# Performance work log

Measured on AMD Instinct MI355X. Metric: run time of the kernel, lower is better.

Reference implementation:

```python
import jax, jax.numpy as jnp
import numpy as np
import math

B, S, E, H, F = 2, 2048, 1024, 16, 4096
D = E // H
EPS = 1e-5


def _layernorm(x, g, b):
    mu = jnp.mean(x, axis=-1, keepdims=True)
    var = jnp.mean(jnp.square(x - mu), axis=-1, keepdims=True)
    return (x - mu) * jax.lax.rsqrt(var + EPS) * g + b


def _xavier(k, fan_in, fan_out):
    limit = math.sqrt(6.0 / (fan_in + fan_out))
    return jax.random.uniform(k, (fan_in, fan_out), jnp.float32, -limit, limit)


def setup_inputs() -> dict:
    key = jax.random.key(0)
    ks = jax.random.split(key, 8)
    x = jax.random.normal(ks[0], (B, S, E), jnp.float32)
    # causal mask: 1 where attendable, 0 where masked (masked_fill at mask==0)
    mask = jnp.tril(jnp.ones((S, S), jnp.int32))[None, None]  # [1,1,S,S]
    return {
        "x": x,
        "mask": mask,
        "Wq": _xavier(ks[1], E, E), "bq": jnp.zeros((E,), jnp.float32),
        "Wk": _xavier(ks[2], E, E), "bk": jnp.zeros((E,), jnp.float32),
        "Wv": _xavier(ks[3], E, E), "bv": jnp.zeros((E,), jnp.float32),
        "Wo": _xavier(ks[4], E, E), "bo": jnp.zeros((E,), jnp.float32),
        "W1": _xavier(ks[5], E, F), "b1": jnp.zeros((F,), jnp.float32),
        "W2": _xavier(ks[6], F, E), "b2": jnp.zeros((E,), jnp.float32),
        "ln1_g": jnp.ones((E,), jnp.float32), "ln1_b": jnp.zeros((E,), jnp.float32),
        "ln2_g": jnp.ones((E,), jnp.float32), "ln2_b": jnp.zeros((E,), jnp.float32),
    }


def reference(x, mask, Wq, bq, Wk, bk, Wv, bv, Wo, bo, W1, b1, W2, b2,
              ln1_g, ln1_b, ln2_g, ln2_b):
    n = _layernorm(x, ln1_g, ln1_b)
    # project and split heads: [B,S,E] -> [B,H,S,D]
    def heads(w, b):
        return (n @ w + b).reshape(B, S, H, D).transpose(0, 2, 1, 3)
    Q, K, V = heads(Wq, bq), heads(Wk, bk), heads(Wv, bv)
    scores = jnp.einsum('bhsd,bhtd->bhst', Q, K) / math.sqrt(D)  # [B,H,S,S]
    scores = jnp.where(mask == 0, jnp.float32(-1e9), scores)
    attn = jax.nn.softmax(scores, axis=-1)
    ctx = jnp.einsum('bhst,bhtd->bhsd', attn, V)
    ctx = ctx.transpose(0, 2, 1, 3).reshape(B, S, E)
    attn_out = ctx @ Wo + bo
    x = _layernorm(x + attn_out, ln2_g, ln2_b)
    ffn = jax.nn.gelu(x @ W1 + b1, approximate=False) @ W2 + b2
    return x + ffn
```

## Files before the change

kernel.cpp:

```cpp
#include <hip/hip_runtime.h>
#include <cmath>

typedef unsigned short u16;
typedef unsigned int u32;
typedef __bf16 bf16x8 __attribute__((ext_vector_type(8)));
typedef float f32x4 __attribute__((ext_vector_type(4)));

#define SEQ 2048
#define EMB 1024
#define NHEAD 16
#define HDIM 64
#define FFDIM 4096
#define NBATCH 2
#define QKVLD 3072
#define PWS 68

#define QSCALE 0.18033688011112042f

__device__ __forceinline__ u16 f2bf(float f) {
  u32 u = __float_as_uint(f);
  u32 r = u + 0x7fffu + ((u >> 16) & 1u);
  return (u16)(r >> 16);
}

__device__ __forceinline__ float ex2(float x) {
#if __has_builtin(__builtin_amdgcn_exp2f)
  return __builtin_amdgcn_exp2f(x);
#else
  return exp2f(x);
#endif
}

__device__ __forceinline__ float geluf(float x) {
  float u = 0.7978845608028654f * (x + 0.044715f * x * x * x);
  float e = ex2(2.8853900817779268f * u);
  return x - x / (e + 1.0f);
}

__device__ __forceinline__ void gload16(const void* g, void* l) {
  __builtin_amdgcn_global_load_lds(
      (const __attribute__((address_space(1))) unsigned int*)g,
      (__attribute__((address_space(3))) unsigned int*)l, 16, 0, 0);
}

__device__ __forceinline__ u32 lds_addr(const void* p) {
  return (u32)(size_t)(const __attribute__((address_space(3))) void*)p;
}

template <int IMM>
__device__ __forceinline__ bf16x8 dsr16(u32 a) {
  bf16x8 r;
  asm volatile("ds_read_b128 %0, %1 offset:%2" : "=v"(r) : "v"(a), "n"(IMM));
  return r;
}

__device__ __forceinline__ void xcd_swizzle(int gx, int gy, int& bx, int& by) {
  int nwg = gx * gy;
  int lin = blockIdx.x + gx * blockIdx.y;
  int q = nwg >> 3;
  int nl = (lin & 7) * q + (lin >> 3);
  bx = nl % gx;
  by = nl / gx;
}

template <int TX>
__device__ __forceinline__ void xcd_tile_swizzle(int gx, int gy, int& bx, int& by) {
  int nwg = gx * gy;
  int lin = blockIdx.x + gx * blockIdx.y;
  int c = lin & 7;
  int wdx = lin >> 3;
  int q = nwg >> 3;
  int TY = q / TX;
  int ncx = gx / TX;
  int xt = c % ncx, yt = c / ncx;
  bx = xt * TX + wdx % TX;
  by = yt * TY + wdx / TX;
}

__global__ __launch_bounds__(256)
void wtrans_kernel(const float* __restrict__ W, u16* __restrict__ WT, int K, int N) {
  __shared__ float tile[32][33];
  int tx = threadIdx.x & 31, ty = threadIdx.x >> 5;
  int n0 = blockIdx.x * 32, k0 = blockIdx.y * 32;
#pragma unroll
  for (int i = 0; i < 32; i += 8)
    tile[ty + i][tx] = W[(size_t)(k0 + ty + i) * N + (n0 + tx)];
  __syncthreads();
#pragma unroll
  for (int i = 0; i < 32; i += 8)
    WT[(size_t)(n0 + ty + i) * K + (k0 + tx)] = f2bf(tile[tx][ty + i]);
}

__global__ __launch_bounds__(256)
void wtrans4_kernel(const float* __restrict__ W0, const float* __restrict__ W1_,
                    const float* __restrict__ W2_, const float* __restrict__ W3,
                    u16* __restrict__ Dqkv, u16* __restrict__ Do) {
  __shared__ float tile[32][33];
  int z = blockIdx.z;
  const float* W = (z == 0) ? W0 : (z == 1) ? W1_ : (z == 2) ? W2_ : W3;
  u16* D = (z < 3) ? (Dqkv + (size_t)z * EMB * EMB) : Do;
  int tx = threadIdx.x & 31, ty = threadIdx.x >> 5;
  int n0 = blockIdx.x * 32, k0 = blockIdx.y * 32;
#pragma unroll
  for (int i = 0; i < 32; i += 8)
    tile[ty + i][tx] = W[(size_t)(k0 + ty + i) * EMB + (n0 + tx)];
  __syncthreads();
#pragma unroll
  for (int i = 0; i < 32; i += 8)
    D[(size_t)(n0 + ty + i) * EMB + (k0 + tx)] = f2bf(tile[tx][ty + i]);
}

__global__ __launch_bounds__(256)
void vtrans_kernel(const u16* __restrict__ QKV, u16* __restrict__ Vt) {
  __shared__ u16 tile[64 * 72];
  int bh = blockIdx.y, b = bh >> 4, h = bh & 15;
  int s0 = blockIdx.x * 64;
  const u16* src = QKV + (size_t)b * SEQ * QKVLD + 2048 + (size_t)h * HDIM;
  int tid = threadIdx.x;
#pragma unroll
  for (int cc = 0; cc < 2; ++cc) {
    int c = tid + cc * 256;
    int s = c >> 3, d0 = (c & 7) * 8;
    uint4 v = *(const uint4*)(src + (size_t)(s0 + s) * QKVLD + d0);
    *(uint4*)(&tile[s * 72 + d0]) = v;
  }
  __syncthreads();
  u16* dst = Vt + (size_t)bh * HDIM * SEQ;
#pragma unroll
  for (int cc = 0; cc < 2; ++cc) {
    int c = tid + cc * 256;
    int d = c >> 3, t0l = (c & 7) * 8;
    union { uint4 u; u16 s[8]; } ou;
#pragma unroll
    for (int j = 0; j < 8; ++j) ou.s[j] = tile[(t0l + j) * 72 + d];
    *(uint4*)(dst + (size_t)d * SEQ + s0 + t0l) = ou.u;
  }
}

__global__ __launch_bounds__(256)
void ln_kernel(const float* __restrict__ in, const float* __restrict__ gamma,
               const float* __restrict__ beta, u16* __restrict__ outb) {
  int w = threadIdx.x >> 6, lane = threadIdx.x & 63;
  int row = blockIdx.x * 4 + w;
  size_t base = (size_t)row * EMB;
  float4 v[4];
  float s = 0.f, q = 0.f;
#pragma unroll
  for (int j = 0; j < 4; ++j) {
    v[j] = *(const float4*)(in + base + j * 256 + lane * 4);
    s += v[j].x + v[j].y + v[j].z + v[j].w;
    q += v[j].x * v[j].x + v[j].y * v[j].y + v[j].z * v[j].z + v[j].w * v[j].w;
  }
#pragma unroll
  for (int off = 1; off < 64; off <<= 1) {
    s += __shfl_xor(s, off);
    q += __shfl_xor(q, off);
  }
  float mean = s * (1.0f / EMB);
  float var = q * (1.0f / EMB) - mean * mean;
  float rstd = rsqrtf(var + 1e-5f);
#pragma unroll
  for (int j = 0; j < 4; ++j) {
    int c = j * 256 + lane * 4;
    float4 g4 = *(const float4*)(gamma + c);
    float4 b4 = *(const float4*)(beta + c);
    ushort4 ob;
    ob.x = f2bf((v[j].x - mean) * rstd * g4.x + b4.x);
    ob.y = f2bf((v[j].y - mean) * rstd * g4.y + b4.y);
    ob.z = f2bf((v[j].z - mean) * rstd * g4.z + b4.z);
    ob.w = f2bf((v[j].w - mean) * rstd * g4.w + b4.w);
    *(ushort4*)(outb + base + c) = ob;
  }
}

__global__ __launch_bounds__(256)
void ln2f_kernel(const float* __restrict__ p, size_t pstride,
                 const float* __restrict__ bias, const float* __restrict__ resid,
                 const float* __restrict__ gamma, const float* __restrict__ beta,
                 u16* __restrict__ outb, float* __restrict__ outf) {
  int w = threadIdx.x >> 6, lane = threadIdx.x & 63;
  int row = blockIdx.x * 4 + w;
  size_t base = (size_t)row * EMB;
  float4 v[4];
  float s = 0.f, q = 0.f;
#pragma unroll
  for (int j = 0; j < 4; ++j) {
    int c = j * 256 + lane * 4;
    float4 a = *(const float4*)(p + base + c);
    float4 b = *(const float4*)(p + pstride + base + c);
    float4 r = *(const float4*)(resid + base + c);
    float4 bb = *(const float4*)(bias + c);
    v[j].x = a.x + b.x + r.x + bb.x;
    v[j].y = a.y + b.y + r.y + bb.y;
    v[j].z = a.z + b.z + r.z + bb.z;
    v[j].w = a.w + b.w + r.w + bb.w;
    s += v[j].x + v[j].y + v[j].z + v[j].w;
    q += v[j].x * v[j].x + v[j].y * v[j].y + v[j].z * v[j].z + v[j].w * v[j].w;
  }
#pragma unroll
  for (int off = 1; off < 64; off <<= 1) {
    s += __shfl_xor(s, off);
    q += __shfl_xor(q, off);
  }
  float mean = s * (1.0f / EMB);
  float var = q * (1.0f / EMB) - mean * mean;
  float rstd = rsqrtf(var + 1e-5f);
#pragma unroll
  for (int j = 0; j < 4; ++j) {
    int c = j * 256 + lane * 4;
    float4 g4 = *(const float4*)(gamma + c);
    float4 b4 = *(const float4*)(beta + c);
    float y0 = (v[j].x - mean) * rstd * g4.x + b4.x;
    float y1 = (v[j].y - mean) * rstd * g4.y + b4.y;
    float y2 = (v[j].z - mean) * rstd * g4.z + b4.z;
    float y3 = (v[j].w - mean) * rstd * g4.w + b4.w;
    ushort4 ob;
    ob.x = f2bf(y0); ob.y = f2bf(y1); ob.z = f2bf(y2); ob.w = f2bf(y3);
    *(ushort4*)(outb + base + c) = ob;
    *(float4*)(outf + base + c) = make_float4(y0, y1, y2, y3);
  }
}

__global__ __launch_bounds__(256)
void reduce2_kernel(const float* __restrict__ p, size_t pstride,
                    const float* __restrict__ bias, const float* __restrict__ resid,
                    float* __restrict__ out, int ncols) {
  size_t i = ((size_t)blockIdx.x * 256 + threadIdx.x) * 4;
  float4 a = *(const float4*)(p + i);
  float4 b = *(const float4*)(p + pstride + i);
  float4 r = *(const float4*)(resid + i);
  int col = (int)(i & (size_t)(ncols - 1));
  float4 bb = *(const float4*)(bias + col);
  float4 o;
  o.x = a.x + b.x + r.x + bb.x;
  o.y = a.y + b.y + r.y + bb.y;
  o.z = a.z + b.z + r.z + bb.z;
  o.w = a.w + b.w + r.w + bb.w;
  *(float4*)(out + i) = o;
}

__global__ __launch_bounds__(256)
void gemm_bt(const u16* __restrict__ A, const u16* __restrict__ BT,
             const float* __restrict__ bias, const float* __restrict__ bias2,
             const float* __restrict__ bias3, void* __restrict__ out,
             const float* __restrict__ resid, int M, int N, int K,
             int mode, float scale, int ksplit,
             float* __restrict__ partial, size_t pstride) {
  __shared__ __align__(16) u16 As[128 * 64];
  __shared__ __align__(16) u16 Bs[128 * 64];
  int tid = threadIdx.x;
  int lane = tid & 63, w = tid >> 6;
  int wm = w >> 1, wn = w & 1;
  int g = lane >> 4, lr = lane & 15;
  int bx, by;
  xcd_swizzle(gridDim.x, gridDim.y, bx, by);
  int m0 = by * 128, n0 = bx * 128;
  int z = blockIdx.z;
  int kbeg = z * ksplit, kend = kbeg + ksplit;

  f32x4 acc[4][4];
#pragma unroll
  for (int mt = 0; mt < 4; ++mt)
#pragma unroll
    for (int nt = 0; nt < 4; ++nt) {
      acc[mt][nt][0] = 0.f; acc[mt][nt][1] = 0.f;
      acc[mt][nt][2] = 0.f; acc[mt][nt][3] = 0.f;
    }

  size_t ao[4], bo_[4];
  int lo[4];
#pragma unroll
  for (int cc = 0; cc < 4; ++cc) {
    int c = tid + cc * 256;
    int row = c >> 3, slot = c & 7;
    int gc = slot ^ (row & 7);
    ao[cc] = (size_t)(m0 + row) * K + gc * 8;
    bo_[cc] = (size_t)(n0 + row) * K + gc * 8;
    lo[cc] = c * 8;
  }
  int swz[2];
#pragma unroll
  for (int kk = 0; kk < 2; ++kk) swz[kk] = ((kk * 4 + g) ^ (lr & 7)) * 8;

  for (int k0 = kbeg; k0 < kend; k0 += 64) {
    __syncthreads();
#pragma unroll
    for (int cc = 0; cc < 4; ++cc) gload16(A + ao[cc] + k0, As + lo[cc]);
#pragma unroll
    for (int cc = 0; cc < 4; ++cc) gload16(BT + bo_[cc] + k0, Bs + lo[cc]);
    __syncthreads();
#pragma unroll
    for (int kk = 0; kk < 2; ++kk) {
      bf16x8 af[4], bfr[4];
#pragma unroll
      for (int mt = 0; mt < 4; ++mt)
        af[mt] = *(const bf16x8*)(As + (wm * 64 + mt * 16 + lr) * 64 + swz[kk]);
#pragma unroll
      for (int nt = 0; nt < 4; ++nt)
        bfr[nt] = *(const bf16x8*)(Bs + (wn * 64 + nt * 16 + lr) * 64 + swz[kk]);
#pragma unroll
      for (int mt = 0; mt < 4; ++mt)
#pragma unroll
        for (int nt = 0; nt < 4; ++nt)
          acc[mt][nt] = __builtin_amdgcn_mfma_f32_16x16x32_bf16(af[mt], bfr[nt], acc[mt][nt], 0, 0, 0);
    }
  }

  float* pz = partial + (size_t)z * pstride;
#pragma unroll
  for (int mt = 0; mt < 4; ++mt) {
    int row = m0 + wm * 64 + mt * 16 + g * 4;
#pragma unroll
    for (int nt = 0; nt < 4; ++nt) {
      int col = n0 + wn * 64 + nt * 16 + lr;
      float bcol;
      if (mode == 3) {
        int which = col >> 10;
        const float* bp = (which == 0) ? bias : (which == 1) ? bias2 : bias3;
        bcol = bp[col & 1023];
      } else if (mode != 4) {
        bcol = bias[col];
      } else {
        bcol = 0.f;
      }
#pragma unroll
      for (int r = 0; r < 4; ++r) {
        float vacc = acc[mt][nt][r] + bcol;
        size_t idx = (size_t)(row + r) * N + col;
        if (mode == 0)      ((u16*)out)[idx] = f2bf(vacc * scale);
        else if (mode == 1) ((u16*)out)[idx] = f2bf(geluf(vacc));
        else if (mode == 2) ((float*)out)[idx] = vacc + resid[idx];
        else if (mode == 3) ((u16*)out)[idx] = f2bf(col < 1024 ? vacc * QSCALE : vacc);
        else                pz[idx] = vacc;
      }
    }
  }
}


#define BARM __builtin_amdgcn_s_barrier()
#define VMW6 asm volatile("s_waitcnt vmcnt(6)")
#define VMW0 asm volatile("s_waitcnt vmcnt(0)")
#define NOSTG ((void)0)
#define NOWT ((void)0)
#define NABUF (128 * 32)

#define STGN_A(t, d, kh)                                                      \
  { gload16(A + (size_t)sgA[0] + kbeg + (t) * 64 + (kh) * 32,                 \
            As + ((d) * 2 + (kh)) * NABUF + sl[0]);                           \
    gload16(A + (size_t)sgA[1] + kbeg + (t) * 64 + (kh) * 32,                 \
            As + ((d) * 2 + (kh)) * NABUF + sl[1]); }

#define STGN_B(t, d, kh)                                                      \
  { gload16(BT + (size_t)sgB[0] + kbeg + (t) * 64 + (kh) * 32,                \
            Bs + ((d) * 2 + (kh)) * NABUF + sl[0]);                           \
    gload16(BT + (size_t)sgB[1] + kbeg + (t) * 64 + (kh) * 32,                \
            Bs + ((d) * 2 + (kh)) * NABUF + sl[1]); }

#define PHASEN(d, kk, mh, STAGE, WAITC)                                       \
  {                                                                           \
    const u32 bA = bB + ((d) * 2 + (kk)) * (NABUF * 2);                       \
    const u32 aA = aB + ((d) * 2 + (kk)) * (NABUF * 2);                       \
    if ((mh) == 0) {                                                          \
      bfr[0] = dsr16<0>(bA);                                                  \
      bfr[1] = dsr16<1024>(bA);                                               \
      bfr[2] = dsr16<2048>(bA);                                               \
      bfr[3] = dsr16<3072>(bA);                                               \
    }                                                                         \
    bf16x8 af[2];                                                             \
    af[0] = dsr16<(((mh) * 2 + 0) * 1024)>(aA);                               \
    af[1] = dsr16<(((mh) * 2 + 1) * 1024)>(aA);                               \
    STAGE;                                                                    \
    BARM;                                                                     \
    asm volatile("s_waitcnt lgkmcnt(0)");                                     \
    __builtin_amdgcn_sched_barrier(0);                                        \
    __builtin_amdgcn_s_setprio(1);                                            \
    _Pragma("unroll")                                                         \
    for (int mi = 0; mi < 2; ++mi)                                            \
      _Pragma("unroll")                                                       \
      for (int nt = 0; nt < 4; ++nt)                                          \
        acc[(mh) * 2 + mi][nt] = __builtin_amdgcn_mfma_f32_16x16x32_bf16(     \
            af[mi], bfr[nt], acc[(mh) * 2 + mi][nt], 0, 0, 0);                \
    __builtin_amdgcn_s_setprio(0);                                            \
    WAITC;                                                                    \
    BARM;                                                                     \
  }

template <int TXS>
__global__ __launch_bounds__(256, 2)
void gemm8n(const u16* __restrict__ A, const u16* __restrict__ BT,
            const float* __restrict__ bias, const float* __restrict__ bias2,
            const float* __restrict__ bias3, void* __restrict__ out,
            const float* __restrict__ resid, int M, int N, int K,
            int mode, float scale, int ksplit,
            float* __restrict__ partial, size_t pstride) {
  __shared__ __align__(16) u16 As[4 * NABUF];
  __shared__ __align__(16) u16 Bs[4 * NABUF];
  int tid = threadIdx.x;
  int lane = tid & 63, w = tid >> 6;
  int wm = w >> 1, wn = w & 1;
  int g = lane >> 4, lr = lane & 15;
  int bx, by;
  xcd_tile_swizzle<TXS>(gridDim.x, gridDim.y, bx, by);
  int m0 = by * 128, n0 = bx * 128;
  int z = blockIdx.z;
  size_t kbeg = (size_t)z * ksplit;
  int nk = ksplit >> 6, npair = nk >> 1;

  int phys = ((lr & 1) * 4 + g) ^ ((lr >> 1) & 7);
  int aoff = wm * 64 * 32 + (lr >> 1) * 64 + phys * 8;
  int boff = wn * 64 * 32 + (lr >> 1) * 64 + phys * 8;
  const u32 aB = lds_addr(As) + 2 * aoff;
  const u32 bB = lds_addr(Bs) + 2 * boff;

  int sgA[2], sgB[2], sl[2];
#pragma unroll
  for (int j = 0; j < 2; ++j) {
    int c = tid + j * 256;
    int sr = c >> 3, ph = c & 7, l = ph ^ (sr & 7);
    sgA[j] = (m0 + 2 * sr + (l >> 2)) * K + (l & 3) * 8;
    sgB[j] = (n0 + 2 * sr + (l >> 2)) * K + (l & 3) * 8;
    sl[j] = c * 8;
  }

  f32x4 acc[4][4];
#pragma unroll
  for (int mt = 0; mt < 4; ++mt)
#pragma unroll
    for (int nt = 0; nt < 4; ++nt) {
      acc[mt][nt][0] = 0.f; acc[mt][nt][1] = 0.f;
      acc[mt][nt][2] = 0.f; acc[mt][nt][3] = 0.f;
    }

  bf16x8 bfr[4];

  STGN_B(0, 0, 0); STGN_A(0, 0, 0); STGN_B(0, 0, 1); STGN_A(0, 0, 1);
  STGN_B(1, 1, 0); STGN_A(1, 1, 0); STGN_B(1, 1, 1);
  VMW6; BARM;

  for (int it = 0; it < npair - 1; ++it) {
    int t1 = 2 * it + 1, t2 = 2 * it + 2, t3 = 2 * it + 3;
    PHASEN(0, 0, 0, STGN_A(t1, 1, 1), NOWT)
    PHASEN(0, 0, 1, STGN_B(t2, 0, 0), NOWT)
    PHASEN(0, 1, 0, STGN_A(t2, 0, 0), NOWT)
    PHASEN(0, 1, 1, STGN_B(t2, 0, 1), VMW6)
    PHASEN(1, 0, 0, STGN_A(t2, 0, 1), NOWT)
    PHASEN(1, 0, 1, STGN_B(t3, 1, 0), NOWT)
    PHASEN(1, 1, 0, STGN_A(t3, 1, 0), NOWT)
    PHASEN(1, 1, 1, STGN_B(t3, 1, 1), VMW6)
  }
  {
    int t1 = nk - 1;
    PHASEN(0, 0, 0, STGN_A(t1, 1, 1), NOWT)
    PHASEN(0, 0, 1, NOSTG, NOWT)
    PHASEN(0, 1, 0, NOSTG, NOWT)
    PHASEN(0, 1, 1, NOSTG, VMW0)
    PHASEN(1, 0, 0, NOSTG, NOWT)
    PHASEN(1, 0, 1, NOSTG, NOWT)
    PHASEN(1, 1, 0, NOSTG, NOWT)
    PHASEN(1, 1, 1, NOSTG, NOWT)
  }

  float* pz = partial + (size_t)z * pstride;
#pragma unroll
  for (int mt = 0; mt < 4; ++mt) {
    int row = m0 + wm * 64 + mt * 16 + g * 4;
#pragma unroll
    for (int nt = 0; nt < 4; ++nt) {
      int col = n0 + wn * 64 + nt * 16 + lr;
      float bcol;
      if (mode == 3) {
        int which = col >> 10;
        const float* bp = (which == 0) ? bias : (which == 1) ? bias2 : bias3;
        bcol = bp[col & 1023];
      } else if (mode != 4) {
        bcol = bias[col];
      } else {
        bcol = 0.f;
      }
#pragma unroll
      for (int r = 0; r < 4; ++r) {
        float vacc = acc[mt][nt][r] + bcol;
        size_t idx = (size_t)(row + r) * N + col;
        if (mode == 0)      ((u16*)out)[idx] = f2bf(vacc * scale);
        else if (mode == 1) ((u16*)out)[idx] = f2bf(geluf(vacc));
        else if (mode == 2) ((float*)out)[idx] = vacc + resid[idx];
        else if (mode == 3) ((u16*)out)[idx] = f2bf(col < 1024 ? vacc * QSCALE : vacc);
        else                pz[idx] = vacc;
      }
    }
  }
}

__shared__ __align__(16) u16 attn_Kt[64 * 64];
__shared__ __align__(16) u16 attn_VT[64 * 64];
__shared__ __align__(16) u16 attn_Pw[2][4][16 * PWS];

template <int S0>
__device__ __forceinline__ void attn_tile(
    int t0, const int* q0, int w, int g, int lr, const bf16x8& ones,
    bf16x8 (&qf)[2][2], f32x4 (&lacc)[2], f32x4 (&oacc)[2][4]) {
  f32x4 sacc[2][4];
#pragma unroll
  for (int s = S0; s < 2; ++s)
#pragma unroll
    for (int nt = 0; nt < 4; ++nt) {
      sacc[s][nt][0] = 0.f; sacc[s][nt][1] = 0.f;
      sacc[s][nt][2] = 0.f; sacc[s][nt][3] = 0.f;
    }
#pragma unroll
  for (int kk = 0; kk < 2; ++kk)
#pragma unroll
    for (int nt = 0; nt < 4; ++nt) {
      int sw = ((kk * 4 + g) ^ lr) & 7;
      bf16x8 bfr = *(const bf16x8*)(&attn_Kt[(nt * 16 + lr) * 64 + sw * 8]);
      if (S0 == 0)
        sacc[0][nt] = __builtin_amdgcn_mfma_f32_16x16x32_bf16(qf[0][kk], bfr, sacc[0][nt], 0, 0, 0);
      sacc[1][nt] = __builtin_amdgcn_mfma_f32_16x16x32_bf16(qf[1][kk], bfr, sacc[1][nt], 0, 0, 0);
    }

#pragma unroll
  for (int s = S0; s < 2; ++s) {
    bool diag = (t0 == q0[s]);
#pragma unroll
    for (int r = 0; r < 4; ++r) {
#pragma unroll
      for (int nt = 0; nt < 4; ++nt) {
        float pv = ex2(sacc[s][nt][r]);
        if (diag && (nt * 16 + lr > w * 16 + g * 4 + r)) pv = 0.f;
        attn_Pw[s][w][(g * 4 + r) * PWS + nt * 16 + lr] = f2bf(pv);
      }
    }
  }

#pragma unroll
  for (int kk = 0; kk < 2; ++kk) {
    bf16x8 pf0, pf1;
    if (S0 == 0) pf0 = *(const bf16x8*)(&attn_Pw[0][w][lr * PWS + kk * 32 + g * 8]);
    pf1 = *(const bf16x8*)(&attn_Pw[1][w][lr * PWS + kk * 32 + g * 8]);
#pragma unroll
    for (int nt = 0; nt < 4; ++nt) {
      int sw = ((kk * 4 + g) ^ lr) & 7;
      bf16x8 vf = *(const bf16x8*)(&attn_VT[(nt * 16 + lr) * 64 + sw * 8]);
      if (S0 == 0)
        oacc[0][nt] = __builtin_amdgcn_mfma_f32_16x16x32_bf16(pf0, vf, oacc[0][nt], 0, 0, 0);
      oacc[1][nt] = __builtin_amdgcn_mfma_f32_16x16x32_bf16(pf1, vf, oacc[1][nt], 0, 0, 0);
    }
    if (S0 == 0)
      lacc[0] = __builtin_amdgcn_mfma_f32_16x16x32_bf16(pf0, ones, lacc[0], 0, 0, 0);
    lacc[1] = __builtin_amdgcn_mfma_f32_16x16x32_bf16(pf1, ones, lacc[1], 0, 0, 0);
  }
}

__global__ __launch_bounds__(256)
void attn2_kernel(const u16* __restrict__ QKV, const u16* __restrict__ Vt,
                  u16* __restrict__ ctx) {
  int tid = threadIdx.x, lane = tid & 63, w = tid >> 6;
  int g = lane >> 4, lr = lane & 15;
  int bh = blockIdx.y, b = bh >> 4, h = bh & 15;
  int q0[2];
  q0[0] = blockIdx.x * 64;
  q0[1] = (SEQ / 64 - 1 - blockIdx.x) * 64;
  const u16* Qh = QKV + (size_t)b * SEQ * QKVLD + (size_t)h * HDIM;
  const u16* Kh = Qh + 1024;
  const u16* Vth = Vt + (size_t)bh * HDIM * SEQ;

  bf16x8 ones;
#pragma unroll
  for (int j = 0; j < 8; ++j) ones[j] = (__bf16)1.0f;

  bf16x8 qf[2][2];
#pragma unroll
  for (int s = 0; s < 2; ++s)
#pragma unroll
    for (int kk = 0; kk < 2; ++kk)
      qf[s][kk] = *(const bf16x8*)(Qh + (size_t)(q0[s] + w * 16 + lr) * QKVLD + kk * 32 + g * 8);

  f32x4 lacc[2];
  f32x4 oacc[2][4];
#pragma unroll
  for (int s = 0; s < 2; ++s) {
    lacc[s][0] = 0.f; lacc[s][1] = 0.f; lacc[s][2] = 0.f; lacc[s][3] = 0.f;
#pragma unroll
    for (int nt = 0; nt < 4; ++nt) {
      oacc[s][nt][0] = 0.f; oacc[s][nt][1] = 0.f;
      oacc[s][nt][2] = 0.f; oacc[s][nt][3] = 0.f;
    }
  }

  int c1 = tid, c2 = tid + 256;
  int t1 = c1 >> 3, ch1 = (c1 ^ t1) & 7;
  int t2 = c2 >> 3, ch2 = (c2 ^ t2) & 7;
  for (int t0 = 0; t0 <= q0[1]; t0 += 64) {
    __syncthreads();
    gload16(Kh + (size_t)(t0 + t1) * QKVLD + ch1 * 8, attn_Kt + c1 * 8);
    gload16(Kh + (size_t)(t0 + t2) * QKVLD + ch2 * 8, attn_Kt + c2 * 8);
    gload16(Vth + (size_t)t1 * SEQ + t0 + ch1 * 8, attn_VT + c1 * 8);
    gload16(Vth + (size_t)t2 * SEQ + t0 + ch2 * 8, attn_VT + c2 * 8);
    __syncthreads();

    if (t0 <= q0[0])
      attn_tile<0>(t0, q0, w, g, lr, ones, qf, lacc, oacc);
    else
      attn_tile<1>(t0, q0, w, g, lr, ones, qf, lacc, oacc);
  }

#pragma unroll
  for (int s = 0; s < 2; ++s) {
    int srow = q0[s] + w * 16 + g * 4;
    float inv[4];
#pragma unroll
    for (int r = 0; r < 4; ++r) inv[r] = 1.0f / lacc[s][r];
#pragma unroll
    for (int nt = 0; nt < 4; ++nt) {
      int col = h * HDIM + nt * 16 + lr;
#pragma unroll
      for (int r = 0; r < 4; ++r) {
        float o = oacc[s][nt][r] * inv[r];
        ctx[((size_t)b * SEQ + srow + r) * EMB + col] = f2bf(o);
      }
    }
  }
}

extern "C" void kernel_launch(void* const* d_in, const int* in_sizes, int n_in,
                              void* d_out, int out_size, void* d_ws, size_t ws_size,
                              hipStream_t stream) {
  const float* x    = (const float*)d_in[0];
  const float* Wq   = (const float*)d_in[2];
  const float* bq   = (const float*)d_in[3];
  const float* Wk   = (const float*)d_in[4];
  const float* bk   = (const float*)d_in[5];
  const float* Wv   = (const float*)d_in[6];
  const float* bv   = (const float*)d_in[7];
  const float* Wo   = (const float*)d_in[8];
  const float* bo   = (const float*)d_in[9];
  const float* W1   = (const float*)d_in[10];
  const float* b1   = (const float*)d_in[11];
  const float* W2   = (const float*)d_in[12];
  const float* b2   = (const float*)d_in[13];
  const float* ln1g = (const float*)d_in[14];
  const float* ln1b = (const float*)d_in[15];
  const float* ln2g = (const float*)d_in[16];
  const float* ln2b = (const float*)d_in[17];

  char* ws = (char*)d_ws;
  u16* WqkvT = (u16*)(ws + ((size_t)0 << 20));
  u16* WoT   = (u16*)(ws + ((size_t)6 << 20));
  u16* W1T   = (u16*)(ws + ((size_t)8 << 20));
  u16* W2T   = (u16*)(ws + ((size_t)16 << 20));
  u16* xb    = (u16*)(ws + ((size_t)24 << 20));
  u16* QKVb  = (u16*)(ws + ((size_t)32 << 20));
  u16* ctxb  = (u16*)(ws + ((size_t)56 << 20));
  float* x2f = (float*)(ws + ((size_t)48 << 20));
  u16* x2b   = xb;
  u16* VtG   = (u16*)(ws + ((size_t)64 << 20));
  float* pWo = (float*)(ws + ((size_t)64 << 20));
  u16* h1    = (u16*)(ws + ((size_t)64 << 20));
  float* pF2 = (float*)(ws + ((size_t)0 << 20));

  dim3 blk(256);
  const int M = NBATCH * SEQ;

  wtrans4_kernel<<<dim3(32, 32, 4), blk, 0, stream>>>(Wq, Wk, Wv, Wo, WqkvT, WoT);
  wtrans_kernel<<<dim3(128, 32), blk, 0, stream>>>(W1, W1T, EMB, FFDIM);
  wtrans_kernel<<<dim3(32, 128), blk, 0, stream>>>(W2, W2T, FFDIM, EMB);

  ln_kernel<<<M / 4, blk, 0, stream>>>(x, ln1g, ln1b, xb);

  gemm_bt<<<dim3(QKVLD / 128, M / 128), blk, 0, stream>>>(
      xb, WqkvT, bq, bk, bv, QKVb, nullptr, M, QKVLD, EMB, 3, 1.0f, EMB, nullptr, 0);

  vtrans_kernel<<<dim3(SEQ / 64, NBATCH * NHEAD), blk, 0, stream>>>(QKVb, VtG);

  attn2_kernel<<<dim3(SEQ / 128, NBATCH * NHEAD), blk, 0, stream>>>(QKVb, VtG, ctxb);

  gemm8n<4><<<dim3(EMB / 128, M / 128, 2), blk, 0, stream>>>(
      ctxb, WoT, nullptr, nullptr, nullptr, nullptr, nullptr, M, EMB, EMB, 4, 1.0f,
      EMB / 2, pWo, (size_t)4 << 20);

  ln2f_kernel<<<M / 4, blk, 0, stream>>>(pWo, (size_t)4 << 20, bo, x, ln2g, ln2b,
                                         x2b, x2f);

  gemm8n<8><<<dim3(FFDIM / 128, M / 128), blk, 0, stream>>>(
      x2b, W1T, b1, nullptr, nullptr, h1, nullptr, M, FFDIM, EMB, 1, 1.0f, EMB,
      nullptr, 0);

  gemm8n<4><<<dim3(EMB / 128, M / 128, 2), blk, 0, stream>>>(
      h1, W2T, nullptr, nullptr, nullptr, nullptr, nullptr, M, EMB, FFDIM, 4, 1.0f,
      FFDIM / 2, pF2, (size_t)8 << 20);
  reduce2_kernel<<<M * EMB / 1024, blk, 0, stream>>>(pF2, (size_t)8 << 20, b2, x2f,
                                                     (float*)d_out, EMB);
}
```

Baseline: 404.9 us.

## Replace 128x128 GEMM with 512-thread 256-wide tile GEMM and coarser phases

Replaces the 256-thread 128x128 gemm8n with a templated 512-thread gemm4p using 128x256 or 256x256 output tiles and 8 waves. Each phase now loads all A fragments and computes the full per-wave tile, so there are four barrier phases per k-pair instead of eight. The goal is more reuse per LDS byte and fewer barriers for the Wo, FFN1 and FFN2 GEMMs. In exchange, grids get smaller and use plain xcd_swizzle instead of the tile swizzle. LDS use and register pressure also rise (64 accumulators per wave at BM=256), which may cut occupancy and wave counts.

```diff
diff --git a/kernel.cpp b/kernel.cpp
--- a/kernel.cpp
+++ b/kernel.cpp
@@ -61,20 +61,6 @@
   int nl = (lin & 7) * q + (lin >> 3);
   bx = nl % gx;
   by = nl / gx;
-}
-
-template <int TX>
-__device__ __forceinline__ void xcd_tile_swizzle(int gx, int gy, int& bx, int& by) {
-  int nwg = gx * gy;
-  int lin = blockIdx.x + gx * blockIdx.y;
-  int c = lin & 7;
-  int wdx = lin >> 3;
-  int q = nwg >> 3;
-  int TY = q / TX;
-  int ncx = gx / TX;
-  int xt = c % ncx, yt = c / ncx;
-  bx = xt * TX + wdx % TX;
-  by = yt * TY + wdx / TX;
 }
 
 __global__ __launch_bounds__(256)
@@ -339,93 +325,112 @@
 
 
 #define BARM __builtin_amdgcn_s_barrier()
-#define VMW6 asm volatile("s_waitcnt vmcnt(6)")
-#define VMW0 asm volatile("s_waitcnt vmcnt(0)")
 #define NOSTG ((void)0)
 #define NOWT ((void)0)
-#define NABUF (128 * 32)
-
-#define STGN_A(t, d, kh)                                                      \
-  { gload16(A + (size_t)sgA[0] + kbeg + (t) * 64 + (kh) * 32,                 \
-            As + ((d) * 2 + (kh)) * NABUF + sl[0]);                           \
-    gload16(A + (size_t)sgA[1] + kbeg + (t) * 64 + (kh) * 32,                 \
-            As + ((d) * 2 + (kh)) * NABUF + sl[1]); }
-
-#define STGN_B(t, d, kh)                                                      \
-  { gload16(BT + (size_t)sgB[0] + kbeg + (t) * 64 + (kh) * 32,                \
-            Bs + ((d) * 2 + (kh)) * NABUF + sl[0]);                           \
-    gload16(BT + (size_t)sgB[1] + kbeg + (t) * 64 + (kh) * 32,                \
-            Bs + ((d) * 2 + (kh)) * NABUF + sl[1]); }
-
-#define PHASEN(d, kk, mh, STAGE, WAITC)                                       \
+
+#define STG_A(t, d, kh)                                                       \
+  { _Pragma("unroll")                                                         \
+    for (int j = 0; j < RA; ++j)                                              \
+      gload16(A + (size_t)sgA[j] + kbeg + (t) * 64 + (kh) * 32,               \
+              As + ((d) * 2 + (kh)) * ABUF + slA[j]); }
+
+#define STG_B(t, d, kh)                                                       \
+  { _Pragma("unroll")                                                         \
+    for (int j = 0; j < 2; ++j)                                               \
+      gload16(BT + (size_t)sgB[j] + kbeg + (t) * 64 + (kh) * 32,              \
+              Bs + ((d) * 2 + (kh)) * 8192 + slB[j]); }
+
+#define STG_R(t, d, kh) { STG_B(t, d, kh); STG_A(t, d, kh); }
+
+#define VM2L asm volatile("s_waitcnt vmcnt(%0)" ::"n"(2 * (RA + 2)))
+#define VM1L asm volatile("s_waitcnt vmcnt(%0)" ::"n"(RA + 2))
+#define VMW0 asm volatile("s_waitcnt vmcnt(0)")
+
+#define PHASE4(d, kk, STAGE, WAITC)                                           \
   {                                                                           \
-    const u32 bA = bB + ((d) * 2 + (kk)) * (NABUF * 2);                       \
-    const u32 aA = aB + ((d) * 2 + (kk)) * (NABUF * 2);                       \
-    if ((mh) == 0) {                                                          \
-      bfr[0] = dsr16<0>(bA);                                                  \
-      bfr[1] = dsr16<1024>(bA);                                               \
-      bfr[2] = dsr16<2048>(bA);                                               \
-      bfr[3] = dsr16<3072>(bA);                                               \
+    const u32 bA = bB + ((d) * 2 + (kk)) * 16384;                             \
+    const u32 aA = aB + ((d) * 2 + (kk)) * (ABUF * 2);                        \
+    bfr[0] = dsr16<0>(bA);                                                    \
+    bfr[1] = dsr16<1024>(bA);                                                 \
+    bfr[2] = dsr16<2048>(bA);                                                 \
+    bfr[3] = dsr16<3072>(bA);                                                 \
+    bf16x8 af[MT];                                                            \
+    af[0] = dsr16<0>(aA);                                                     \
+    af[1] = dsr16<1024>(aA);                                                  \
+    af[2] = dsr16<2048>(aA);                                                  \
+    af[3] = dsr16<3072>(aA);                                                  \
+    if constexpr (MT > 4) {                                                   \
+      af[4] = dsr16<4096>(aA);                                                \
+      af[5] = dsr16<5120>(aA);                                                \
+      af[6] = dsr16<6144>(aA);                                                \
+      af[7] = dsr16<7168>(aA);                                                \
     }                                                                         \
-    bf16x8 af[2];                                                             \
-    af[0] = dsr16<(((mh) * 2 + 0) * 1024)>(aA);                               \
-    af[1] = dsr16<(((mh) * 2 + 1) * 1024)>(aA);                               \
     STAGE;                                                                    \
-    BARM;                                                                     \
     asm volatile("s_waitcnt lgkmcnt(0)");                                     \
     __builtin_amdgcn_sched_barrier(0);                                        \
     __builtin_amdgcn_s_setprio(1);                                            \
     _Pragma("unroll")                                                         \
-    for (int mi = 0; mi < 2; ++mi)                                            \
+    for (int mi = 0; mi < MT; ++mi)                                           \
       _Pragma("unroll")                                                       \
       for (int nt = 0; nt < 4; ++nt)                                          \
-        acc[(mh) * 2 + mi][nt] = __builtin_amdgcn_mfma_f32_16x16x32_bf16(     \
-            af[mi], bfr[nt], acc[(mh) * 2 + mi][nt], 0, 0, 0);                \
+        acc[mi][nt] = __builtin_amdgcn_mfma_f32_16x16x32_bf16(                \
+            af[mi], bfr[nt], acc[mi][nt], 0, 0, 0);                           \
     __builtin_amdgcn_s_setprio(0);                                            \
     WAITC;                                                                    \
     BARM;                                                                     \
   }
 
-template <int TXS>
-__global__ __launch_bounds__(256, 2)
-void gemm8n(const u16* __restrict__ A, const u16* __restrict__ BT,
+template <int BM>
+__global__ __launch_bounds__(512, 2)
+void gemm4p(const u16* __restrict__ A, const u16* __restrict__ BT,
             const float* __restrict__ bias, const float* __restrict__ bias2,
             const float* __restrict__ bias3, void* __restrict__ out,
             const float* __restrict__ resid, int M, int N, int K,
             int mode, float scale, int ksplit,
             float* __restrict__ partial, size_t pstride) {
-  __shared__ __align__(16) u16 As[4 * NABUF];
-  __shared__ __align__(16) u16 Bs[4 * NABUF];
+  constexpr int MT = BM / 32;
+  constexpr int RA = BM / 128;
+  constexpr int ABUF = BM * 32;
+  __shared__ __align__(16) u16 As[4 * ABUF];
+  __shared__ __align__(16) u16 Bs[4 * 8192];
+
   int tid = threadIdx.x;
   int lane = tid & 63, w = tid >> 6;
-  int wm = w >> 1, wn = w & 1;
+  int wm = w >> 2, wn = w & 3;
   int g = lane >> 4, lr = lane & 15;
   int bx, by;
-  xcd_tile_swizzle<TXS>(gridDim.x, gridDim.y, bx, by);
-  int m0 = by * 128, n0 = bx * 128;
+  xcd_swizzle(gridDim.x, gridDim.y, bx, by);
+  int m0 = by * BM, n0 = bx * 256;
   int z = blockIdx.z;
   size_t kbeg = (size_t)z * ksplit;
   int nk = ksplit >> 6, npair = nk >> 1;
 
   int phys = ((lr & 1) * 4 + g) ^ ((lr >> 1) & 7);
-  int aoff = wm * 64 * 32 + (lr >> 1) * 64 + phys * 8;
-  int boff = wn * 64 * 32 + (lr >> 1) * 64 + phys * 8;
+  int aoff = wm * (BM / 2) * 32 + (lr >> 1) * 64 + phys * 8;
+  int boff = wn * 2048 + (lr >> 1) * 64 + phys * 8;
   const u32 aB = lds_addr(As) + 2 * aoff;
   const u32 bB = lds_addr(Bs) + 2 * boff;
 
-  int sgA[2], sgB[2], sl[2];
-#pragma unroll
-  for (int j = 0; j < 2; ++j) {
-    int c = tid + j * 256;
+  int sgA[RA], slA[RA];
+#pragma unroll
+  for (int j = 0; j < RA; ++j) {
+    int c = tid + j * 512;
     int sr = c >> 3, ph = c & 7, l = ph ^ (sr & 7);
     sgA[j] = (m0 + 2 * sr + (l >> 2)) * K + (l & 3) * 8;
+    slA[j] = c * 8;
+  }
+  int sgB[2], slB[2];
+#pragma unroll
+  for (int j = 0; j < 2; ++j) {
+    int c = tid + j * 512;
+    int sr = c >> 3, ph = c & 7, l = ph ^ (sr & 7);
     sgB[j] = (n0 + 2 * sr + (l >> 2)) * K + (l & 3) * 8;
-    sl[j] = c * 8;
-  }
-
-  f32x4 acc[4][4];
-#pragma unroll
-  for (int mt = 0; mt < 4; ++mt)
+    slB[j] = c * 8;
+  }
+
+  f32x4 acc[MT][4];
+#pragma unroll
+  for (int mt = 0; mt < MT; ++mt)
 #pragma unroll
     for (int nt = 0; nt < 4; ++nt) {
       acc[mt][nt][0] = 0.f; acc[mt][nt][1] = 0.f;
@@ -434,37 +439,28 @@
 
   bf16x8 bfr[4];
 
-  STGN_B(0, 0, 0); STGN_A(0, 0, 0); STGN_B(0, 0, 1); STGN_A(0, 0, 1);
-  STGN_B(1, 1, 0); STGN_A(1, 1, 0); STGN_B(1, 1, 1);
-  VMW6; BARM;
+  STG_R(0, 0, 0); STG_R(0, 0, 1); STG_R(1, 1, 0);
+  VM2L; BARM;
 
   for (int it = 0; it < npair - 1; ++it) {
     int t1 = 2 * it + 1, t2 = 2 * it + 2, t3 = 2 * it + 3;
-    PHASEN(0, 0, 0, STGN_A(t1, 1, 1), NOWT)
-    PHASEN(0, 0, 1, STGN_B(t2, 0, 0), NOWT)
-    PHASEN(0, 1, 0, STGN_A(t2, 0, 0), NOWT)
-    PHASEN(0, 1, 1, STGN_B(t2, 0, 1), VMW6)
-    PHASEN(1, 0, 0, STGN_A(t2, 0, 1), NOWT)
-    PHASEN(1, 0, 1, STGN_B(t3, 1, 0), NOWT)
-    PHASEN(1, 1, 0, STGN_A(t3, 1, 0), NOWT)
-    PHASEN(1, 1, 1, STGN_B(t3, 1, 1), VMW6)
+    PHASE4(0, 0, STG_R(t1, 1, 1), VM2L)
+    PHASE4(0, 1, STG_R(t2, 0, 0), VM2L)
+    PHASE4(1, 0, STG_R(t2, 0, 1), VM2L)
+    PHASE4(1, 1, STG_R(t3, 1, 0), VM2L)
   }
   {
     int t1 = nk - 1;
-    PHASEN(0, 0, 0, STGN_A(t1, 1, 1), NOWT)
-    PHASEN(0, 0, 1, NOSTG, NOWT)
-    PHASEN(0, 1, 0, NOSTG, NOWT)
-    PHASEN(0, 1, 1, NOSTG, VMW0)
-    PHASEN(1, 0, 0, NOSTG, NOWT)
-    PHASEN(1, 0, 1, NOSTG, NOWT)
-    PHASEN(1, 1, 0, NOSTG, NOWT)
-    PHASEN(1, 1, 1, NOSTG, NOWT)
+    PHASE4(0, 0, STG_R(t1, 1, 1), VM2L)
+    PHASE4(0, 1, NOSTG, VM1L)
+    PHASE4(1, 0, NOSTG, VMW0)
+    PHASE4(1, 1, NOSTG, NOWT)
   }
 
   float* pz = partial + (size_t)z * pstride;
 #pragma unroll
-  for (int mt = 0; mt < 4; ++mt) {
-    int row = m0 + wm * 64 + mt * 16 + g * 4;
+  for (int mt = 0; mt < MT; ++mt) {
+    int row = m0 + wm * (BM / 2) + mt * 16 + g * 4;
 #pragma unroll
     for (int nt = 0; nt < 4; ++nt) {
       int col = n0 + wn * 64 + nt * 16 + lr;
@@ -660,6 +656,7 @@
   float* pF2 = (float*)(ws + ((size_t)0 << 20));
 
   dim3 blk(256);
+  dim3 blk512(512);
   const int M = NBATCH * SEQ;
 
   wtrans4_kernel<<<dim3(32, 32, 4), blk, 0, stream>>>(Wq, Wk, Wv, Wo, WqkvT, WoT);
@@ -675,18 +672,18 @@
 
   attn2_kernel<<<dim3(SEQ / 128, NBATCH * NHEAD), blk, 0, stream>>>(QKVb, VtG, ctxb);
 
-  gemm8n<4><<<dim3(EMB / 128, M / 128, 2), blk, 0, stream>>>(
+  gemm4p<128><<<dim3(EMB / 256, M / 128, 2), blk512, 0, stream>>>(
       ctxb, WoT, nullptr, nullptr, nullptr, nullptr, nullptr, M, EMB, EMB, 4, 1.0f,
       EMB / 2, pWo, (size_t)4 << 20);
 
   ln2f_kernel<<<M / 4, blk, 0, stream>>>(pWo, (size_t)4 << 20, bo, x, ln2g, ln2b,
                                          x2b, x2f);
 
-  gemm8n<8><<<dim3(FFDIM / 128, M / 128), blk, 0, stream>>>(
+  gemm4p<256><<<dim3(FFDIM / 256, M / 256), blk512, 0, stream>>>(
       x2b, W1T, b1, nullptr, nullptr, h1, nullptr, M, FFDIM, EMB, 1, 1.0f, EMB,
       nullptr, 0);
 
-  gemm8n<4><<<dim3(EMB / 128, M / 128, 2), blk, 0, stream>>>(
+  gemm4p<128><<<dim3(EMB / 256, M / 128, 2), blk512, 0, stream>>>(
       h1, W2T, nullptr, nullptr, nullptr, nullptr, nullptr, M, EMB, FFDIM, 4, 1.0f,
       FFDIM / 2, pF2, (size_t)8 << 20);
   reduce2_kernel<<<M * EMB / 1024, blk, 0, stream>>>(pF2, (size_t)8 << 20, b2, x2f,
```

Result: no change. 397.4 us, median of 2 (-1.9%).
